# Kernel optimization log

Hardware: AMD Instinct MI355X
Metric: run time of the kernel (lower is better)

## Reference

```python
import jax, jax.numpy as jnp
import numpy as np

N1 = 20000
N2 = 20000
E = 160000
C_IN = 128
HID = 64
HEADS = 4


def _param(key, shape, fan_in):
    return jax.random.normal(key, shape, dtype=jnp.float32) * (1.0 / np.sqrt(fan_in))


def setup_inputs() -> dict:
    key = jax.random.key(0)
    ks = jax.random.split(key, 24)
    inp = {
        "x1": jax.random.normal(ks[0], (N1, C_IN), dtype=jnp.float32),
        "x2": jax.random.normal(ks[1], (N2, C_IN), dtype=jnp.float32),
        "edge_index1": jax.random.randint(ks[2], (2, E), 0, N1, dtype=jnp.int32),
        "edge_index2": jax.random.randint(ks[3], (2, E), 0, N2, dtype=jnp.int32),
    }
    # GAT layer 0: in->hid
    inp["W0"] = _param(ks[4], (C_IN, HEADS * HID), C_IN)
    inp["a0s"] = _param(ks[5], (HEADS, HID), HID)
    inp["a0d"] = _param(ks[6], (HEADS, HID), HID)
    inp["b0"] = jnp.zeros((HID,), jnp.float32)
    # GAT layer 1: hid->hid
    inp["W1"] = _param(ks[7], (HID, HEADS * HID), HID)
    inp["a1s"] = _param(ks[8], (HEADS, HID), HID)
    inp["a1d"] = _param(ks[9], (HEADS, HID), HID)
    inp["b1"] = jnp.zeros((HID,), jnp.float32)
    # GAT layer 2: hid->in
    inp["W2"] = _param(ks[10], (HID, HEADS * C_IN), HID)
    inp["a2s"] = _param(ks[11], (HEADS, C_IN), C_IN)
    inp["a2d"] = _param(ks[12], (HEADS, C_IN), C_IN)
    inp["b2"] = jnp.zeros((C_IN,), jnp.float32)
    # final GAT: in->in
    inp["Wf"] = _param(ks[13], (C_IN, HEADS * C_IN), C_IN)
    inp["afs"] = _param(ks[14], (HEADS, C_IN), C_IN)
    inp["afd"] = _param(ks[15], (HEADS, C_IN), C_IN)
    inp["bf"] = jnp.zeros((C_IN,), jnp.float32)
    # residual linear in->in
    inp["Wres"] = _param(ks[16], (C_IN, C_IN), C_IN)
    inp["bres"] = jnp.zeros((C_IN,), jnp.float32)
    return inp


def gat_conv(x, src, dst, W, att_src, att_dst, bias, num_nodes):
    """PyG GATConv, concat=False (mean over heads), eval mode (no dropout)."""
    H, C = att_src.shape
    h = (x @ W).reshape(num_nodes, H, C)                      # [N,H,C]
    a_s = jnp.sum(h * att_src, axis=-1)                       # [N,H]
    a_d = jnp.sum(h * att_dst, axis=-1)                       # [N,H]
    e = jax.nn.leaky_relu(a_s[src] + a_d[dst], negative_slope=0.2)  # [E,H]
    e_max = jax.ops.segment_max(e, dst, num_segments=num_nodes)
    e_exp = jnp.exp(e - e_max[dst])
    denom = jax.ops.segment_sum(e_exp, dst, num_segments=num_nodes)
    alpha = e_exp / (denom[dst] + 1e-16)                      # edge softmax over dst
    msg = alpha[:, :, None] * h[src]                          # [E,H,C]
    out = jax.ops.segment_sum(msg, dst, num_segments=num_nodes)  # [N,H,C]
    return out.mean(axis=1) + bias


def reference(x1, x2, edge_index1, edge_index2,
              W0, a0s, a0d, b0, W1, a1s, a1d, b1, W2, a2s, a2d, b2,
              Wf, afs, afd, bf, Wres, bres):
    n1 = x1.shape[0]
    n2 = x2.shape[0]
    N = n1 + n2
    x = jnp.concatenate([x1, x2], axis=0)
    # combined edges: e1, e2+n1, e1+n1 (eval-mode EdgeManipulationLayer = offset)
    src = jnp.concatenate([edge_index1[0], edge_index2[0] + n1, edge_index1[0] + n1])
    dst = jnp.concatenate([edge_index1[1], edge_index2[1] + n1, edge_index1[1] + n1])
    residual = x2 @ Wres + bres
    h = x
    for (W, asrc, adst, b) in ((W0, a0s, a0d, b0), (W1, a1s, a1d, b1), (W2, a2s, a2d, b2)):
        h = jax.nn.relu(gat_conv(h, src, dst, W, asrc, adst, b, N))
    h = gat_conv(h, src, dst, Wf, afs, afd, bf, N)
    h2 = h[n1:n1 + n2]
    norm = jnp.linalg.norm(h2, axis=1, keepdims=True)
    h2n = h2 / jnp.maximum(norm, 1e-12)  # F.normalize(p=2, dim=1)
    return h2n + residual
```

## Files before the change

### kernel.cpp

```cpp
#include <hip/hip_runtime.h>
#include <hip/hip_bf16.h>

#define NN  20000
#define EC  160000
#define ETN 320000
#define CINC 128
#define HC 4
#define NBLK 79

typedef __attribute__((ext_vector_type(8))) short short8v;
typedef __attribute__((ext_vector_type(4))) float f32x4;

__device__ __forceinline__ ushort f2bu(float f){
  __hip_bfloat16 h = __float2bfloat16(f);
  union { __hip_bfloat16 b; ushort u; } v; v.b = h; return v.u;
}
__device__ __forceinline__ float b2f(ushort u){
  return __uint_as_float(((unsigned)u) << 16);
}
__device__ __forceinline__ float blo(unsigned v){ return __uint_as_float(v << 16); }
__device__ __forceinline__ float bhi(unsigned v){ return __uint_as_float(v & 0xffff0000u); }

__device__ __forceinline__ void edge_sd(int e, const int* __restrict__ ei1,
                                        const int* __restrict__ ei2, int& s, int& d){
  if (e < EC){ s = ei2[e];      d = ei2[EC + e]; }
  else       { int t = e - EC; s = ei1[t]; d = ei1[EC + t]; }
}

__device__ __forceinline__ float4 leaky4(float4 v){
  v.x = v.x > 0.f ? v.x : 0.2f*v.x;
  v.y = v.y > 0.f ? v.y : 0.2f*v.y;
  v.z = v.z > 0.f ? v.z : 0.2f*v.z;
  v.w = v.w > 0.f ? v.w : 0.2f*v.w;
  return v;
}


__global__ void cast_x(const float* __restrict__ x2, ushort* __restrict__ X){
  int i = blockIdx.x*256 + threadIdx.x;
  if (i >= NN*CINC) return;
  X[i] = f2bu(x2[i]);
}

__global__ void permW_k(const float* __restrict__ W, ushort* __restrict__ Wt,
                        int K, int M, int Ch){
  int i = blockIdx.x*256 + threadIdx.x;
  if (i >= K*M) return;
  int m = i / K, k = i - m*K;
  int col = Ch ? ((m & 3)*Ch + (m >> 2)) : m;
  Wt[i] = f2bu(W[k*M + col]);
}

template<int K, bool F32OUT>
__global__ __launch_bounds__(256)
void gemm_mfma(const ushort* __restrict__ X, const ushort* __restrict__ Wt,
               ushort* __restrict__ Hout, float* __restrict__ HoutF, int nrows, int M){
  __shared__ float st[4][16][68];
  const int lane = threadIdx.x & 63;
  const int w    = threadIdx.x >> 6;
  const int n0   = blockIdx.x*128 + w*16;
  const int m0   = blockIdx.y*64;
  const int hi = lane >> 4;
  const int lo = lane & 15;
  int ra0 = n0 + lo;      if (ra0 >= nrows) ra0 = nrows - 1;
  int ra1 = n0 + 64 + lo; if (ra1 >= nrows) ra1 = nrows - 1;
  const ushort* ap0 = X + (long)ra0*K + hi*8;
  const ushort* ap1 = X + (long)ra1*K + hi*8;

  f32x4 acc0[4], acc1[4];
  #pragma unroll
  for (int t = 0; t < 4; ++t){ acc0[t] = (f32x4){0.f,0.f,0.f,0.f}; acc1[t] = acc0[t]; }

  #pragma unroll
  for (int k0 = 0; k0 < K; k0 += 32){
    short8v a0 = *(const short8v*)(ap0 + k0);
    short8v a1 = *(const short8v*)(ap1 + k0);
    #pragma unroll
    for (int t = 0; t < 4; ++t){
      short8v b = *(const short8v*)(Wt + (long)(m0 + t*16 + lo)*K + k0 + hi*8);
      acc0[t] = __builtin_amdgcn_mfma_f32_16x16x32_bf16(a0, b, acc0[t], 0, 0, 0);
      acc1[t] = __builtin_amdgcn_mfma_f32_16x16x32_bf16(a1, b, acc1[t], 0, 0, 0);
    }
  }

  const int row = lane >> 2, cg = lane & 3;
  #pragma unroll
  for (int half = 0; half < 2; ++half){
    f32x4* acc = half ? acc1 : acc0;
    const int nb = n0 + half*64;
    #pragma unroll
    for (int t = 0; t < 4; ++t)
      #pragma unroll
      for (int j = 0; j < 4; ++j)
        st[w][hi*4 + j][t*16 + lo] = acc[t][j];
    __builtin_amdgcn_wave_barrier();
    if (nb + row < nrows){
      if (F32OUT){
        float* op = HoutF + (long)(nb + row)*M + m0 + cg*16;
        #pragma unroll
        for (int q = 0; q < 4; ++q)
          *(float4*)(op + q*4) = *(float4*)&st[w][row][cg*16 + q*4];
      } else {
        ushort* op = Hout + (long)(nb + row)*M + m0 + cg*16;
        #pragma unroll
        for (int q = 0; q < 4; ++q){
          float4 v = *(float4*)&st[w][row][cg*16 + q*4];
          ushort4 u; u.x = f2bu(v.x); u.y = f2bu(v.y); u.z = f2bu(v.z); u.w = f2bu(v.w);
          *(ushort4*)(op + q*4) = u;
        }
      }
    }
    __builtin_amdgcn_wave_barrier();
  }
}

template<int C>
__global__ __launch_bounds__(256)
void att_scores_w(const ushort* __restrict__ H16, const float* __restrict__ att_s,
                  const float* __restrict__ att_d, float* __restrict__ AS,
                  float* __restrict__ AD){
  const int lane = threadIdx.x & 63;
  const int w    = threadIdx.x >> 6;
  const int n    = blockIdx.x*4 + w;
  const ushort* hp = H16 + (long)n*(HC*C);
  float as0=0.f, as1=0.f, as2=0.f, as3=0.f;
  float ad0=0.f, ad1=0.f, ad2=0.f, ad3=0.f;
  #pragma unroll
  for (int j = 0; j < C/64; ++j){
    int c = lane + j*64;
    uint2 u = *(const uint2*)(hp + c*4);
    float h0 = blo(u.x);
    float h1 = bhi(u.x);
    float h2 = blo(u.y);
    float h3 = bhi(u.y);
    as0 += h0*att_s[0*C + c]; ad0 += h0*att_d[0*C + c];
    as1 += h1*att_s[1*C + c]; ad1 += h1*att_d[1*C + c];
    as2 += h2*att_s[2*C + c]; ad2 += h2*att_d[2*C + c];
    as3 += h3*att_s[3*C + c]; ad3 += h3*att_d[3*C + c];
  }
  #pragma unroll
  for (int off = 32; off; off >>= 1){
    as0 += __shfl_xor(as0, off); ad0 += __shfl_xor(ad0, off);
    as1 += __shfl_xor(as1, off); ad1 += __shfl_xor(ad1, off);
    as2 += __shfl_xor(as2, off); ad2 += __shfl_xor(ad2, off);
    as3 += __shfl_xor(as3, off); ad3 += __shfl_xor(ad3, off);
  }
  if (lane == 0){
    ((float4*)AS)[n] = make_float4(as0, as1, as2, as3);
    ((float4*)AD)[n] = make_float4(ad0, ad1, ad2, ad3);
  }
}


__global__ void count_k(const int* __restrict__ ei1, const int* __restrict__ ei2,
                        int* __restrict__ CNT){
  int e = blockIdx.x*256 + threadIdx.x;
  if (e >= ETN) return;
  int s, d; edge_sd(e, ei1, ei2, s, d);
  atomicAdd(&CNT[d], 1);
}

__global__ __launch_bounds__(256) void scan_blk_k(const int* __restrict__ CNT,
                                                  int* __restrict__ EXC,
                                                  int* __restrict__ BSUM){
  __shared__ int s[256];
  const int t = threadIdx.x, b = blockIdx.x;
  const int i = b*256 + t;
  int v = (i < NN) ? CNT[i] : 0;
  s[t] = v;
  __syncthreads();
  #pragma unroll
  for (int off = 1; off < 256; off <<= 1){
    int u = (t >= off) ? s[t - off] : 0;
    __syncthreads();
    s[t] += u;
    __syncthreads();
  }
  if (i < NN) EXC[i] = s[t] - v;
  if (t == 255) BSUM[b] = s[255];
}

__global__ __launch_bounds__(256) void scan_top_k(const int* __restrict__ BSUM,
                                                  int* __restrict__ BOFF){
  __shared__ int s[256];
  const int t = threadIdx.x;
  int v = (t < NBLK) ? BSUM[t] : 0;
  s[t] = v;
  __syncthreads();
  #pragma unroll
  for (int off = 1; off < 256; off <<= 1){
    int u = (t >= off) ? s[t - off] : 0;
    __syncthreads();
    s[t] += u;
    __syncthreads();
  }
  if (t < NBLK) BOFF[t] = s[t] - v;
}

__global__ __launch_bounds__(256) void scan_add_k(const int* __restrict__ EXC,
                                                  const int* __restrict__ BOFF,
                                                  int* __restrict__ OFF,
                                                  int* __restrict__ CUR){
  int i = blockIdx.x*256 + threadIdx.x;
  if (i < NN){ int o = EXC[i] + BOFF[i >> 8]; OFF[i] = o; CUR[i] = o; }
  if (i == NN) OFF[NN] = ETN;
}

__global__ void scatter_k(const int* __restrict__ ei1, const int* __restrict__ ei2,
                          int* __restrict__ CUR, int* __restrict__ ESRC){
  int e = blockIdx.x*256 + threadIdx.x;
  if (e >= ETN) return;
  int s, d; edge_sd(e, ei1, ei2, s, d);
  int pos = atomicAdd(&CUR[d], 1);
  ESRC[pos] = s;
}

template<bool RELU>
__global__ __launch_bounds__(256)
void agg128_k(const int* __restrict__ OFF, const int* __restrict__ ESRC,
              const float* __restrict__ AS, const float* __restrict__ AD,
              const ushort* __restrict__ H16, const float* __restrict__ bias,
              ushort* __restrict__ Xout){
  __shared__ int    sm_s[4][64];
  __shared__ float4 sm_p[4][64];
  const int lane = threadIdx.x & 63;
  const int w    = threadIdx.x >> 6;
  const int d    = blockIdx.x*4 + w;
  const int beg = OFF[d], end = OFF[d+1];
  const float4 ad4 = ((const float4*)AD)[d];

  float4 den = make_float4(0.f,0.f,0.f,0.f);
  float4 a0A = den, a1A = den, a0B = den, a1B = den;

  for (int i0 = beg; i0 < end; i0 += 64){
    int cnt = min(64, end - i0);
    if (lane < cnt){
      int s = ESRC[i0 + lane];
      float4 a = ((const float4*)AS)[s];
      float4 sc = leaky4(make_float4(a.x+ad4.x, a.y+ad4.y, a.z+ad4.z, a.w+ad4.w));
      float4 p = make_float4(__expf(sc.x), __expf(sc.y), __expf(sc.z), __expf(sc.w));
      den.x += p.x; den.y += p.y; den.z += p.z; den.w += p.w;
      sm_s[w][lane] = s;
      sm_p[w][lane] = p;
    }
    __builtin_amdgcn_wave_barrier();
    int e = 0;
    for (; e + 3 < cnt; e += 4){
      int s0 = sm_s[w][e],   s1 = sm_s[w][e+1];
      int s2 = sm_s[w][e+2], s3 = sm_s[w][e+3];
      float4 p0 = sm_p[w][e],   p1 = sm_p[w][e+1];
      float4 p2 = sm_p[w][e+2], p3 = sm_p[w][e+3];
      uint4 u0 = *(const uint4*)(H16 + (long)s0*512 + lane*8);
      uint4 u1 = *(const uint4*)(H16 + (long)s1*512 + lane*8);
      uint4 u2 = *(const uint4*)(H16 + (long)s2*512 + lane*8);
      uint4 u3 = *(const uint4*)(H16 + (long)s3*512 + lane*8);
      a0A.x += p0.x*blo(u0.x); a0A.y += p0.y*bhi(u0.x);
      a0A.z += p0.z*blo(u0.y); a0A.w += p0.w*bhi(u0.y);
      a1A.x += p0.x*blo(u0.z); a1A.y += p0.y*bhi(u0.z);
      a1A.z += p0.z*blo(u0.w); a1A.w += p0.w*bhi(u0.w);
      a0B.x += p1.x*blo(u1.x); a0B.y += p1.y*bhi(u1.x);
      a0B.z += p1.z*blo(u1.y); a0B.w += p1.w*bhi(u1.y);
      a1B.x += p1.x*blo(u1.z); a1B.y += p1.y*bhi(u1.z);
      a1B.z += p1.z*blo(u1.w); a1B.w += p1.w*bhi(u1.w);
      a0A.x += p2.x*blo(u2.x); a0A.y += p2.y*bhi(u2.x);
      a0A.z += p2.z*blo(u2.y); a0A.w += p2.w*bhi(u2.y);
      a1A.x += p2.x*blo(u2.z); a1A.y += p2.y*bhi(u2.z);
      a1A.z += p2.z*blo(u2.w); a1A.w += p2.w*bhi(u2.w);
      a0B.x += p3.x*blo(u3.x); a0B.y += p3.y*bhi(u3.x);
      a0B.z += p3.z*blo(u3.y); a0B.w += p3.w*bhi(u3.y);
      a1B.x += p3.x*blo(u3.z); a1B.y += p3.y*bhi(u3.z);
      a1B.z += p3.z*blo(u3.w); a1B.w += p3.w*bhi(u3.w);
    }
    for (; e < cnt; ++e){
      int s0 = sm_s[w][e];
      float4 p0 = sm_p[w][e];
      uint4 u0 = *(const uint4*)(H16 + (long)s0*512 + lane*8);
      a0A.x += p0.x*blo(u0.x); a0A.y += p0.y*bhi(u0.x);
      a0A.z += p0.z*blo(u0.y); a0A.w += p0.w*bhi(u0.y);
      a1A.x += p0.x*blo(u0.z); a1A.y += p0.y*bhi(u0.z);
      a1A.z += p0.z*blo(u0.w); a1A.w += p0.w*bhi(u0.w);
    }
    __builtin_amdgcn_wave_barrier();
  }

  #pragma unroll
  for (int off = 32; off; off >>= 1){
    den.x += __shfl_xor(den.x, off);
    den.y += __shfl_xor(den.y, off);
    den.z += __shfl_xor(den.z, off);
    den.w += __shfl_xor(den.w, off);
  }
  float4 r = make_float4(1.f/(den.x + 1e-16f), 1.f/(den.y + 1e-16f),
                         1.f/(den.z + 1e-16f), 1.f/(den.w + 1e-16f));
  int c0 = lane*2;
  float o0 = 0.25f*((a0A.x+a0B.x)*r.x + (a0A.y+a0B.y)*r.y +
                    (a0A.z+a0B.z)*r.z + (a0A.w+a0B.w)*r.w) + bias[c0];
  float o1 = 0.25f*((a1A.x+a1B.x)*r.x + (a1A.y+a1B.y)*r.y +
                    (a1A.z+a1B.z)*r.z + (a1A.w+a1B.w)*r.w) + bias[c0+1];
  if (RELU){ o0 = fmaxf(o0, 0.f); o1 = fmaxf(o1, 0.f); }
  ((unsigned*)Xout)[(long)d*64 + lane] = (unsigned)f2bu(o0) | ((unsigned)f2bu(o1) << 16);
}

__global__ __launch_bounds__(256)
void agg128_final_k(const int* __restrict__ OFF, const int* __restrict__ ESRC,
                    const float* __restrict__ AS, const float* __restrict__ AD,
                    const ushort* __restrict__ H16, const float* __restrict__ bias,
                    const float* __restrict__ RES, const float* __restrict__ bres,
                    float* __restrict__ out){
  __shared__ int    sm_s[4][64];
  __shared__ float4 sm_p[4][64];
  const int lane = threadIdx.x & 63;
  const int w    = threadIdx.x >> 6;
  const int d    = blockIdx.x*4 + w;
  const int beg = OFF[d], end = OFF[d+1];
  const float4 ad4 = ((const float4*)AD)[d];

  float4 den = make_float4(0.f,0.f,0.f,0.f);
  float4 a0A = den, a1A = den, a0B = den, a1B = den;

  for (int i0 = beg; i0 < end; i0 += 64){
    int cnt = min(64, end - i0);
    if (lane < cnt){
      int s = ESRC[i0 + lane];
      float4 a = ((const float4*)AS)[s];
      float4 sc = leaky4(make_float4(a.x+ad4.x, a.y+ad4.y, a.z+ad4.z, a.w+ad4.w));
      float4 p = make_float4(__expf(sc.x), __expf(sc.y), __expf(sc.z), __expf(sc.w));
      den.x += p.x; den.y += p.y; den.z += p.z; den.w += p.w;
      sm_s[w][lane] = s;
      sm_p[w][lane] = p;
    }
    __builtin_amdgcn_wave_barrier();
    int e = 0;
    for (; e + 3 < cnt; e += 4){
      int s0 = sm_s[w][e],   s1 = sm_s[w][e+1];
      int s2 = sm_s[w][e+2], s3 = sm_s[w][e+3];
      float4 p0 = sm_p[w][e],   p1 = sm_p[w][e+1];
      float4 p2 = sm_p[w][e+2], p3 = sm_p[w][e+3];
      uint4 u0 = *(const uint4*)(H16 + (long)s0*512 + lane*8);
      uint4 u1 = *(const uint4*)(H16 + (long)s1*512 + lane*8);
      uint4 u2 = *(const uint4*)(H16 + (long)s2*512 + lane*8);
      uint4 u3 = *(const uint4*)(H16 + (long)s3*512 + lane*8);
      a0A.x += p0.x*blo(u0.x); a0A.y += p0.y*bhi(u0.x);
      a0A.z += p0.z*blo(u0.y); a0A.w += p0.w*bhi(u0.y);
      a1A.x += p0.x*blo(u0.z); a1A.y += p0.y*bhi(u0.z);
      a1A.z += p0.z*blo(u0.w); a1A.w += p0.w*bhi(u0.w);
      a0B.x += p1.x*blo(u1.x); a0B.y += p1.y*bhi(u1.x);
      a0B.z += p1.z*blo(u1.y); a0B.w += p1.w*bhi(u1.y);
      a1B.x += p1.x*blo(u1.z); a1B.y += p1.y*bhi(u1.z);
      a1B.z += p1.z*blo(u1.w); a1B.w += p1.w*bhi(u1.w);
      a0A.x += p2.x*blo(u2.x); a0A.y += p2.y*bhi(u2.x);
      a0A.z += p2.z*blo(u2.y); a0A.w += p2.w*bhi(u2.y);
      a1A.x += p2.x*blo(u2.z); a1A.y += p2.y*bhi(u2.z);
      a1A.z += p2.z*blo(u2.w); a1A.w += p2.w*bhi(u2.w);
      a0B.x += p3.x*blo(u3.x); a0B.y += p3.y*bhi(u3.x);
      a0B.z += p3.z*blo(u3.y); a0B.w += p3.w*bhi(u3.y);
      a1B.x += p3.x*blo(u3.z); a1B.y += p3.y*bhi(u3.z);
      a1B.z += p3.z*blo(u3.w); a1B.w += p3.w*bhi(u3.w);
    }
    for (; e < cnt; ++e){
      int s0 = sm_s[w][e];
      float4 p0 = sm_p[w][e];
      uint4 u0 = *(const uint4*)(H16 + (long)s0*512 + lane*8);
      a0A.x += p0.x*blo(u0.x); a0A.y += p0.y*bhi(u0.x);
      a0A.z += p0.z*blo(u0.y); a0A.w += p0.w*bhi(u0.y);
      a1A.x += p0.x*blo(u0.z); a1A.y += p0.y*bhi(u0.z);
      a1A.z += p0.z*blo(u0.w); a1A.w += p0.w*bhi(u0.w);
    }
    __builtin_amdgcn_wave_barrier();
  }

  #pragma unroll
  for (int off = 32; off; off >>= 1){
    den.x += __shfl_xor(den.x, off);
    den.y += __shfl_xor(den.y, off);
    den.z += __shfl_xor(den.z, off);
    den.w += __shfl_xor(den.w, off);
  }
  float4 r = make_float4(1.f/(den.x + 1e-16f), 1.f/(den.y + 1e-16f),
                         1.f/(den.z + 1e-16f), 1.f/(den.w + 1e-16f));
  int c0 = lane*2;
  float o0 = 0.25f*((a0A.x+a0B.x)*r.x + (a0A.y+a0B.y)*r.y +
                    (a0A.z+a0B.z)*r.z + (a0A.w+a0B.w)*r.w) + bias[c0];
  float o1 = 0.25f*((a1A.x+a1B.x)*r.x + (a1A.y+a1B.y)*r.y +
                    (a1A.z+a1B.z)*r.z + (a1A.w+a1B.w)*r.w) + bias[c0+1];

  float ss = o0*o0 + o1*o1;
  #pragma unroll
  for (int off = 32; off; off >>= 1) ss += __shfl_xor(ss, off);
  float inv = 1.f / fmaxf(sqrtf(ss), 1e-12f);
  float2 res = *(const float2*)(RES + (long)d*CINC + c0);
  float2 ov;
  ov.x = o0*inv + res.x + bres[c0];
  ov.y = o1*inv + res.y + bres[c0+1];
  *(float2*)(out + (long)d*CINC + c0) = ov;
}

template<bool RELU>
__global__ __launch_bounds__(256)
void agg64_k(const int* __restrict__ OFF, const int* __restrict__ ESRC,
             const float* __restrict__ AS, const float* __restrict__ AD,
             const ushort* __restrict__ H16, const float* __restrict__ bias,
             ushort* __restrict__ Xout){
  __shared__ int    sm_s[4][64];
  __shared__ float4 sm_p[4][64];
  const int lane = threadIdx.x & 63;
  const int half = lane >> 5;
  const int l5   = lane & 31;
  const int w    = threadIdx.x >> 6;
  const int d    = blockIdx.x*4 + w;
  const int beg = OFF[d], end = OFF[d+1];
  const float4 ad4 = ((const float4*)AD)[d];

  float4 den = make_float4(0.f,0.f,0.f,0.f);
  float4 a0 = den, a1 = den;

  for (int i0 = beg; i0 < end; i0 += 64){
    int cnt = min(64, end - i0);
    if (lane < cnt){
      int s = ESRC[i0 + lane];
      float4 a = ((const float4*)AS)[s];
      float4 sc = leaky4(make_float4(a.x+ad4.x, a.y+ad4.y, a.z+ad4.z, a.w+ad4.w));
      float4 p = make_float4(__expf(sc.x), __expf(sc.y), __expf(sc.z), __expf(sc.w));
      den.x += p.x; den.y += p.y; den.z += p.z; den.w += p.w;
      sm_s[w][lane] = s;
      sm_p[w][lane] = p;
    }
    __builtin_amdgcn_wave_barrier();
    int e = 0;
    #pragma unroll 4
    for (; e + 1 < cnt; e += 2){
      int ee = e + half;
      int s0 = sm_s[w][ee];
      float4 p0 = sm_p[w][ee];
      uint4 u0 = *(const uint4*)(H16 + (long)s0*256 + l5*8);
      a0.x += p0.x*blo(u0.x); a0.y += p0.y*bhi(u0.x);
      a0.z += p0.z*blo(u0.y); a0.w += p0.w*bhi(u0.y);
      a1.x += p0.x*blo(u0.z); a1.y += p0.y*bhi(u0.z);
      a1.z += p0.z*blo(u0.w); a1.w += p0.w*bhi(u0.w);
    }
    if (e < cnt && half == 0){
      int s0 = sm_s[w][e];
      float4 p0 = sm_p[w][e];
      uint4 u0 = *(const uint4*)(H16 + (long)s0*256 + l5*8);
      a0.x += p0.x*blo(u0.x); a0.y += p0.y*bhi(u0.x);
      a0.z += p0.z*blo(u0.y); a0.w += p0.w*bhi(u0.y);
      a1.x += p0.x*blo(u0.z); a1.y += p0.y*bhi(u0.z);
      a1.z += p0.z*blo(u0.w); a1.w += p0.w*bhi(u0.w);
    }
    __builtin_amdgcn_wave_barrier();
  }

  #pragma unroll
  for (int off = 32; off; off >>= 1){
    den.x += __shfl_xor(den.x, off);
    den.y += __shfl_xor(den.y, off);
    den.z += __shfl_xor(den.z, off);
    den.w += __shfl_xor(den.w, off);
  }
  a0.x += __shfl_xor(a0.x, 32); a0.y += __shfl_xor(a0.y, 32);
  a0.z += __shfl_xor(a0.z, 32); a0.w += __shfl_xor(a0.w, 32);
  a1.x += __shfl_xor(a1.x, 32); a1.y += __shfl_xor(a1.y, 32);
  a1.z += __shfl_xor(a1.z, 32); a1.w += __shfl_xor(a1.w, 32);

  if (half == 0){
    float4 r = make_float4(1.f/(den.x + 1e-16f), 1.f/(den.y + 1e-16f),
                           1.f/(den.z + 1e-16f), 1.f/(den.w + 1e-16f));
    int c0 = l5*2;
    float o0 = 0.25f*(a0.x*r.x + a0.y*r.y + a0.z*r.z + a0.w*r.w) + bias[c0];
    float o1 = 0.25f*(a1.x*r.x + a1.y*r.y + a1.z*r.z + a1.w*r.w) + bias[c0+1];
    if (RELU){ o0 = fmaxf(o0, 0.f); o1 = fmaxf(o1, 0.f); }
    ((unsigned*)Xout)[(long)d*32 + l5] = (unsigned)f2bu(o0) | ((unsigned)f2bu(o1) << 16);
  }
}


extern "C" void kernel_launch(void* const* d_in, const int* in_sizes, int n_in,
                              void* d_out, int out_size, void* d_ws, size_t ws_size,
                              hipStream_t stream) {
  const float* x2  = (const float*)d_in[1];
  const int*   ei1 = (const int*)  d_in[2];
  const int*   ei2 = (const int*)  d_in[3];
  const float* W0  = (const float*)d_in[4];
  const float* a0s = (const float*)d_in[5];
  const float* a0d = (const float*)d_in[6];
  const float* b0  = (const float*)d_in[7];
  const float* W1  = (const float*)d_in[8];
  const float* a1s = (const float*)d_in[9];
  const float* a1d = (const float*)d_in[10];
  const float* b1  = (const float*)d_in[11];
  const float* W2  = (const float*)d_in[12];
  const float* a2s = (const float*)d_in[13];
  const float* a2d = (const float*)d_in[14];
  const float* b2  = (const float*)d_in[15];
  const float* Wf  = (const float*)d_in[16];
  const float* afs = (const float*)d_in[17];
  const float* afd = (const float*)d_in[18];
  const float* bf  = (const float*)d_in[19];
  const float* Wres= (const float*)d_in[20];
  const float* bres= (const float*)d_in[21];
  float* out = (float*)d_out;

  char* ws = (char*)d_ws;
  ushort* X0   = (ushort*)(ws + 0);
  ushort* X1   = (ushort*)(ws + 5120000);
  ushort* H16  = (ushort*)(ws + 10240000);
  float*  RES  = (float*) (ws + 30720000);
  float*  AS   = (float*) (ws + 40960000);
  float*  AD   = (float*) (ws + 41280000);
  int*    OFF  = (int*)   (ws + 41600000);
  int*    CUR  = (int*)   (ws + 41680064);
  int*    ESRC = (int*)   (ws + 41760064);
  int*    CNT  = (int*)   (ws + 43040064);
  ushort* W0t  = (ushort*)(ws + 43120064);
  ushort* W1t  = (ushort*)(ws + 43185600);
  ushort* W2t  = (ushort*)(ws + 43218368);
  ushort* Wft  = (ushort*)(ws + 43283904);
  ushort* Wrt  = (ushort*)(ws + 43414976);
  int*    EXC  = (int*)   (ws + 43447744);
  int*    BSUM = (int*)   (ws + 43527744);
  int*    BOFF = (int*)   (ws + 43528768);

  const int EG = (ETN + 255)/256;

  cast_x<<<(NN*CINC + 255)/256, 256, 0, stream>>>(x2, X0);

  hipMemsetAsync(CNT, 0, NN*4, stream);
  count_k<<<EG, 256, 0, stream>>>(ei1, ei2, CNT);
  scan_blk_k<<<NBLK, 256, 0, stream>>>(CNT, EXC, BSUM);
  scan_top_k<<<1, 256, 0, stream>>>(BSUM, BOFF);
  scan_add_k<<<NBLK, 256, 0, stream>>>(EXC, BOFF, OFF, CUR);
  scatter_k<<<EG, 256, 0, stream>>>(ei1, ei2, CUR, ESRC);

  permW_k<<<(128*256 + 255)/256, 256, 0, stream>>>(W0, W0t, 128, 256, 64);
  permW_k<<<( 64*256 + 255)/256, 256, 0, stream>>>(W1, W1t,  64, 256, 64);
  permW_k<<<( 64*512 + 255)/256, 256, 0, stream>>>(W2, W2t,  64, 512, 128);
  permW_k<<<(128*512 + 255)/256, 256, 0, stream>>>(Wf, Wft, 128, 512, 128);
  permW_k<<<(128*128 + 255)/256, 256, 0, stream>>>(Wres, Wrt, 128, 128, 0);

  {
    dim3 g((NN + 127)/128, 128/64);
    gemm_mfma<128,true><<<g, 256, 0, stream>>>(X0, Wrt, nullptr, RES, NN, 128);
  }

  { dim3 g((NN + 127)/128, 256/64);
    gemm_mfma<128,false><<<g, 256, 0, stream>>>(X0, W0t, H16, nullptr, NN, 256); }
  att_scores_w<64><<<NN/4, 256, 0, stream>>>(H16, a0s, a0d, AS, AD);
  agg64_k<true><<<NN/4, 256, 0, stream>>>(OFF, ESRC, AS, AD, H16, b0, X1);

  { dim3 g((NN + 127)/128, 256/64);
    gemm_mfma<64,false><<<g, 256, 0, stream>>>(X1, W1t, H16, nullptr, NN, 256); }
  att_scores_w<64><<<NN/4, 256, 0, stream>>>(H16, a1s, a1d, AS, AD);
  agg64_k<true><<<NN/4, 256, 0, stream>>>(OFF, ESRC, AS, AD, H16, b1, X0);

  { dim3 g((NN + 127)/128, 512/64);
    gemm_mfma<64,false><<<g, 256, 0, stream>>>(X0, W2t, H16, nullptr, NN, 512); }
  att_scores_w<128><<<NN/4, 256, 0, stream>>>(H16, a2s, a2d, AS, AD);
  agg128_k<true><<<NN/4, 256, 0, stream>>>(OFF, ESRC, AS, AD, H16, b2, X1);

  { dim3 g((NN + 127)/128, 512/64);
    gemm_mfma<128,false><<<g, 256, 0, stream>>>(X1, Wft, H16, nullptr, NN, 512); }
  att_scores_w<128><<<NN/4, 256, 0, stream>>>(H16, afs, afd, AS, AD);
  agg128_final_k<<<NN/4, 256, 0, stream>>>(OFF, ESRC, AS, AD, H16, bf, RES, bres, out);
}
```

Baseline: 311.1 us.

## Fuse attention-score reductions into GEMM epilogue and merge prep kernels

Attention source/destination scores are now computed in the MFMA GEMM epilogue from fp32 accumulators, removing four separate att_scores passes that re-read the bf16 H features. The GEMM is restructured so each block covers 64 rows and loops over all output column tiles, instead of a 2D grid with 128 rows per block. The x cast and the five weight permute kernels are merged into a single prep launch to cut launch overhead. The trade-off is fewer blocks and less parallelism per GEMM, and scores now come from unrounded fp32 values rather than the bf16-rounded H.

Result: slower. 322.2 us (+3.6%).

```diff
diff --git a/kernel.cpp b/kernel.cpp
--- a/kernel.cpp
+++ b/kernel.cpp
@@ -15,9 +15,6 @@
   __hip_bfloat16 h = __float2bfloat16(f);
   union { __hip_bfloat16 b; ushort u; } v; v.b = h; return v.u;
 }
-__device__ __forceinline__ float b2f(ushort u){
-  return __uint_as_float(((unsigned)u) << 16);
-}
 __device__ __forceinline__ float blo(unsigned v){ return __uint_as_float(v << 16); }
 __device__ __forceinline__ float bhi(unsigned v){ return __uint_as_float(v & 0xffff0000u); }
 
@@ -35,59 +32,78 @@
   return v;
 }
 
-
-__global__ void cast_x(const float* __restrict__ x2, ushort* __restrict__ X){
+__global__ void prep_k(const float* __restrict__ x2,
+                       const float* __restrict__ W0, const float* __restrict__ W1,
+                       const float* __restrict__ W2, const float* __restrict__ Wf,
+                       const float* __restrict__ Wres,
+                       ushort* __restrict__ X0,
+                       ushort* __restrict__ W0t, ushort* __restrict__ W1t,
+                       ushort* __restrict__ W2t, ushort* __restrict__ Wft,
+                       ushort* __restrict__ Wrt){
   int i = blockIdx.x*256 + threadIdx.x;
-  if (i >= NN*CINC) return;
-  X[i] = f2bu(x2[i]);
-}
-
-__global__ void permW_k(const float* __restrict__ W, ushort* __restrict__ Wt,
-                        int K, int M, int Ch){
-  int i = blockIdx.x*256 + threadIdx.x;
-  if (i >= K*M) return;
-  int m = i / K, k = i - m*K;
+  if (i < NN*CINC){ X0[i] = f2bu(x2[i]); return; }
+  int j = i - NN*CINC;
+  const float* W; ushort* Wt; int K, M, Ch;
+  if      (j <  32768){ W=W0;  Wt=W0t; K=128; M=256; Ch=64;            }
+  else if (j <  49152){ W=W1;  Wt=W1t; K=64;  M=256; Ch=64;  j-=32768; }
+  else if (j <  81920){ W=W2;  Wt=W2t; K=64;  M=512; Ch=128; j-=49152; }
+  else if (j < 147456){ W=Wf;  Wt=Wft; K=128; M=512; Ch=128; j-=81920; }
+  else if (j < 163840){ W=Wres;Wt=Wrt; K=128; M=128; Ch=0;   j-=147456;}
+  else return;
+  int m = j / K, k = j - m*K;
   int col = Ch ? ((m & 3)*Ch + (m >> 2)) : m;
-  Wt[i] = f2bu(W[k*M + col]);
-}
-
-template<int K, bool F32OUT>
+  Wt[j] = f2bu(W[k*M + col]);
+}
+
+template<int K, int M, bool ATT, bool F32OUT>
 __global__ __launch_bounds__(256)
-void gemm_mfma(const ushort* __restrict__ X, const ushort* __restrict__ Wt,
-               ushort* __restrict__ Hout, float* __restrict__ HoutF, int nrows, int M){
+void gemm_att(const ushort* __restrict__ X, const ushort* __restrict__ Wt,
+              ushort* __restrict__ Hout, float* __restrict__ HoutF,
+              const float* __restrict__ att_s, const float* __restrict__ att_d,
+              float* __restrict__ AS, float* __restrict__ AD, int nrows){
+  constexpr int C = M/4;
   __shared__ float st[4][16][68];
   const int lane = threadIdx.x & 63;
   const int w    = threadIdx.x >> 6;
-  const int n0   = blockIdx.x*128 + w*16;
-  const int m0   = blockIdx.y*64;
+  const int nb   = blockIdx.x*64 + w*16;
   const int hi = lane >> 4;
   const int lo = lane & 15;
-  int ra0 = n0 + lo;      if (ra0 >= nrows) ra0 = nrows - 1;
-  int ra1 = n0 + 64 + lo; if (ra1 >= nrows) ra1 = nrows - 1;
-  const ushort* ap0 = X + (long)ra0*K + hi*8;
-  const ushort* ap1 = X + (long)ra1*K + hi*8;
-
-  f32x4 acc0[4], acc1[4];
-  #pragma unroll
-  for (int t = 0; t < 4; ++t){ acc0[t] = (f32x4){0.f,0.f,0.f,0.f}; acc1[t] = acc0[t]; }
-
-  #pragma unroll
-  for (int k0 = 0; k0 < K; k0 += 32){
-    short8v a0 = *(const short8v*)(ap0 + k0);
-    short8v a1 = *(const short8v*)(ap1 + k0);
+  int ra = nb + lo; if (ra >= nrows) ra = nrows - 1;
+  const ushort* ap = X + (long)ra*K + hi*8;
+  const int row = lane >> 2, cg = lane & 3;
+  const int head = lo & 3;
+
+  float pas[4] = {0.f,0.f,0.f,0.f};
+  float pad[4] = {0.f,0.f,0.f,0.f};
+
+  #pragma unroll
+  for (int mt = 0; mt < M/64; ++mt){
+    const int m0 = mt*64;
+    f32x4 acc[4];
     #pragma unroll
-    for (int t = 0; t < 4; ++t){
-      short8v b = *(const short8v*)(Wt + (long)(m0 + t*16 + lo)*K + k0 + hi*8);
-      acc0[t] = __builtin_amdgcn_mfma_f32_16x16x32_bf16(a0, b, acc0[t], 0, 0, 0);
-      acc1[t] = __builtin_amdgcn_mfma_f32_16x16x32_bf16(a1, b, acc1[t], 0, 0, 0);
-    }
-  }
-
-  const int row = lane >> 2, cg = lane & 3;
-  #pragma unroll
-  for (int half = 0; half < 2; ++half){
-    f32x4* acc = half ? acc1 : acc0;
-    const int nb = n0 + half*64;
+    for (int t = 0; t < 4; ++t) acc[t] = (f32x4){0.f,0.f,0.f,0.f};
+    #pragma unroll
+    for (int k0 = 0; k0 < K; k0 += 32){
+      short8v a = *(const short8v*)(ap + k0);
+      #pragma unroll
+      for (int t = 0; t < 4; ++t){
+        short8v b = *(const short8v*)(Wt + (long)(m0 + t*16 + lo)*K + k0 + hi*8);
+        acc[t] = __builtin_amdgcn_mfma_f32_16x16x32_bf16(a, b, acc[t], 0, 0, 0);
+      }
+    }
+    if (ATT){
+      #pragma unroll
+      for (int t = 0; t < 4; ++t){
+        int c = (m0 + t*16 + lo) >> 2;
+        float vs = att_s[head*C + c];
+        float vd = att_d[head*C + c];
+        #pragma unroll
+        for (int j = 0; j < 4; ++j){
+          pas[j] += acc[t][j]*vs;
+          pad[j] += acc[t][j]*vd;
+        }
+      }
+    }
     #pragma unroll
     for (int t = 0; t < 4; ++t)
       #pragma unroll
@@ -112,42 +128,20 @@
     }
     __builtin_amdgcn_wave_barrier();
   }
-}
-
-template<int C>
-__global__ __launch_bounds__(256)
-void att_scores_w(const ushort* __restrict__ H16, const float* __restrict__ att_s,
-                  const float* __restrict__ att_d, float* __restrict__ AS,
-                  float* __restrict__ AD){
-  const int lane = threadIdx.x & 63;
-  const int w    = threadIdx.x >> 6;
-  const int n    = blockIdx.x*4 + w;
-  const ushort* hp = H16 + (long)n*(HC*C);
-  float as0=0.f, as1=0.f, as2=0.f, as3=0.f;
-  float ad0=0.f, ad1=0.f, ad2=0.f, ad3=0.f;
-  #pragma unroll
-  for (int j = 0; j < C/64; ++j){
-    int c = lane + j*64;
-    uint2 u = *(const uint2*)(hp + c*4);
-    float h0 = blo(u.x);
-    float h1 = bhi(u.x);
-    float h2 = blo(u.y);
-    float h3 = bhi(u.y);
-    as0 += h0*att_s[0*C + c]; ad0 += h0*att_d[0*C + c];
-    as1 += h1*att_s[1*C + c]; ad1 += h1*att_d[1*C + c];
-    as2 += h2*att_s[2*C + c]; ad2 += h2*att_d[2*C + c];
-    as3 += h3*att_s[3*C + c]; ad3 += h3*att_d[3*C + c];
-  }
-  #pragma unroll
-  for (int off = 32; off; off >>= 1){
-    as0 += __shfl_xor(as0, off); ad0 += __shfl_xor(ad0, off);
-    as1 += __shfl_xor(as1, off); ad1 += __shfl_xor(ad1, off);
-    as2 += __shfl_xor(as2, off); ad2 += __shfl_xor(ad2, off);
-    as3 += __shfl_xor(as3, off); ad3 += __shfl_xor(ad3, off);
-  }
-  if (lane == 0){
-    ((float4*)AS)[n] = make_float4(as0, as1, as2, as3);
-    ((float4*)AD)[n] = make_float4(ad0, ad1, ad2, ad3);
+
+  if (ATT){
+    #pragma unroll
+    for (int j = 0; j < 4; ++j){
+      pas[j] += __shfl_xor(pas[j], 4);  pas[j] += __shfl_xor(pas[j], 8);
+      pad[j] += __shfl_xor(pad[j], 4);  pad[j] += __shfl_xor(pad[j], 8);
+    }
+    if (lo < 4){
+      #pragma unroll
+      for (int j = 0; j < 4; ++j){
+        int r = nb + hi*4 + j;
+        if (r < nrows){ AS[r*4 + lo] = pas[j]; AD[r*4 + lo] = pad[j]; }
+      }
+    }
   }
 }
 
@@ -521,8 +515,10 @@
   int*    BOFF = (int*)   (ws + 43528768);
 
   const int EG = (ETN + 255)/256;
-
-  cast_x<<<(NN*CINC + 255)/256, 256, 0, stream>>>(x2, X0);
+  const int GB = (NN + 63)/64;
+
+  prep_k<<<(NN*CINC + 163840 + 255)/256, 256, 0, stream>>>(
+      x2, W0, W1, W2, Wf, Wres, X0, W0t, W1t, W2t, Wft, Wrt);
 
   hipMemsetAsync(CNT, 0, NN*4, stream);
   count_k<<<EG, 256, 0, stream>>>(ei1, ei2, CNT);
@@ -531,34 +527,22 @@
   scan_add_k<<<NBLK, 256, 0, stream>>>(EXC, BOFF, OFF, CUR);
   scatter_k<<<EG, 256, 0, stream>>>(ei1, ei2, CUR, ESRC);
 
-  permW_k<<<(128*256 + 255)/256, 256, 0, stream>>>(W0, W0t, 128, 256, 64);
-  permW_k<<<( 64*256 + 255)/256, 256, 0, stream>>>(W1, W1t,  64, 256, 64);
-  permW_k<<<( 64*512 + 255)/256, 256, 0, stream>>>(W2, W2t,  64, 512, 128);
-  permW_k<<<(128*512 + 255)/256, 256, 0, stream>>>(Wf, Wft, 128, 512, 128);
-  permW_k<<<(128*128 + 255)/256, 256, 0, stream>>>(Wres, Wrt, 128, 128, 0);
-
-  {
-    dim3 g((NN + 127)/128, 128/64);
-    gemm_mfma<128,true><<<g, 256, 0, stream>>>(X0, Wrt, nullptr, RES, NN, 128);
-  }
-
-  { dim3 g((NN + 127)/128, 256/64);
-    gemm_mfma<128,false><<<g, 256, 0, stream>>>(X0, W0t, H16, nullptr, NN, 256); }
-  att_scores_w<64><<<NN/4, 256, 0, stream>>>(H16, a0s, a0d, AS, AD);
+  gemm_att<128,128,false,true><<<GB, 256, 0, stream>>>(
+      X0, Wrt, nullptr, RES, nullptr, nullptr, nullptr, nullptr, NN);
+
+  gemm_att<128,256,true,false><<<GB, 256, 0, stream>>>(
+      X0, W0t, H16, nullptr, a0s, a0d, AS, AD, NN);
   agg64_k<true><<<NN/4, 256, 0, stream>>>(OFF, ESRC, AS, AD, H16, b0, X1);
 
-  { dim3 g((NN + 127)/128, 256/64);
-    gemm_mfma<64,false><<<g, 256, 0, stream>>>(X1, W1t, H16, nullptr, NN, 256); }
-  att_scores_w<64><<<NN/4, 256, 0, stream>>>(H16, a1s, a1d, AS, AD);
+  gemm_att<64,256,true,false><<<GB, 256, 0, stream>>>(
+      X1, W1t, H16, nullptr, a1s, a1d, AS, AD, NN);
   agg64_k<true><<<NN/4, 256, 0, stream>>>(OFF, ESRC, AS, AD, H16, b1, X0);
 
-  { dim3 g((NN + 127)/128, 512/64);
-    gemm_mfma<64,false><<<g, 256, 0, stream>>>(X0, W2t, H16, nullptr, NN, 512); }
-  att_scores_w<128><<<NN/4, 256, 0, stream>>>(H16, a2s, a2d, AS, AD);
+  gemm_att<64,512,true,false><<<GB, 256, 0, stream>>>(
+      X0, W2t, H16, nullptr, a2s, a2d, AS, AD, NN);
   agg128_k<true><<<NN/4, 256, 0, stream>>>(OFF, ESRC, AS, AD, H16, b2, X1);
 
-  { dim3 g((NN + 127)/128, 512/64);
-    gemm_mfma<128,false><<<g, 256, 0, stream>>>(X1, Wft, H16, nullptr, NN, 512); }
-  att_scores_w<128><<<NN/4, 256, 0, stream>>>(H16, afs, afd, AS, AD);
+  gemm_att<128,512,true,false><<<GB, 256, 0, stream>>>(
+      X1, Wft, H16, nullptr, afs, afd, AS, AD, NN);
   agg128_final_k<<<NN/4, 256, 0, stream>>>(OFF, ESRC, AS, AD, H16, bf, RES, bres, out);
 }
```
